# Optimization experiments

Hardware: AMD Instinct MI355X
Metric: run time of the kernel (lower is better)

## Reference

```python
import jax, jax.numpy as jnp
import numpy as np

B, N_BOX, N_THING, ROI = 2, 32, 4, 28
H, W = 768, 704
N_STUFF = 6
N_CLS = N_STUFF + N_THING  # 10
NEG = -100.0


def setup_inputs() -> dict:
    key = jax.random.key(0)
    k1, k2, k3, k4 = jax.random.split(key, 4)
    sem_logits = jax.random.normal(k1, (B, N_CLS, H, W), jnp.float32)
    roi_msk_logits = jax.random.normal(k2, (B, N_BOX, N_THING, ROI, ROI), jnp.float32)
    cls = jax.random.randint(k3, (B, N_BOX), 0, N_THING, jnp.int32)
    u = jax.random.uniform(k4, (B, N_BOX, 4), jnp.float32)
    y0 = u[..., 0] * (H - 80.0)
    x0 = u[..., 1] * (W - 80.0)
    y1 = jnp.minimum(y0 + 32.0 + u[..., 2] * (H / 3.0), H - 1.0)
    x1 = jnp.minimum(x0 + 32.0 + u[..., 3] * (W / 3.0), W - 1.0)
    bbx = jnp.stack([y0, x0, y1, x1], axis=-1)  # (y_min, x_min, y_max, x_max)
    img_size = jnp.array([H, W], jnp.int32)
    return {"sem_logits": sem_logits, "roi_msk_logits": roi_msk_logits,
            "bbx": bbx, "cls": cls, "img_size": img_size}


def _bilinear_paste(msk, bbx, img_size, Hs, Ws):
    # msk: [B,N,R,R]; per-box bilinear resize (align_corners=False) to (h,w) and paste
    # into a [B,N,Hs,Ws] canvas filled with -100, clipped to the image.
    R = msk.shape[-1]
    ref = jnp.floor(bbx).astype(jnp.int32)  # torch .long()/int() truncation (boxes >= 0)
    y0, x0, y1, x1 = ref[..., 0], ref[..., 1], ref[..., 2], ref[..., 3]
    h = jnp.maximum(y1 - y0 + 1, 1).astype(jnp.float32)
    w = jnp.maximum(x1 - x0 + 1, 1).astype(jnp.float32)
    yy = jnp.arange(Hs, dtype=jnp.float32)[None, None, :]          # [1,1,H]
    sy = jnp.clip((yy - y0[..., None] + 0.5) * (R / h)[..., None] - 0.5, 0.0, R - 1.0)
    ylo = jnp.floor(sy).astype(jnp.int32)
    yhi = jnp.minimum(ylo + 1, R - 1)
    wy = sy - ylo                                                   # [B,N,H]
    xx = jnp.arange(Ws, dtype=jnp.float32)[None, None, :]
    sx = jnp.clip((xx - x0[..., None] + 0.5) * (R / w)[..., None] - 0.5, 0.0, R - 1.0)
    xlo = jnp.floor(sx).astype(jnp.int32)
    xhi = jnp.minimum(xlo + 1, R - 1)
    wx = sx - xlo                                                   # [B,N,W]
    rows = (jnp.take_along_axis(msk, ylo[..., None], axis=2) * (1.0 - wy[..., None])
            + jnp.take_along_axis(msk, yhi[..., None], axis=2) * wy[..., None])  # [B,N,H,R]
    up = (jnp.take_along_axis(rows, xlo[:, :, None, :], axis=3) * (1.0 - wx[:, :, None, :])
          + jnp.take_along_axis(rows, xhi[:, :, None, :], axis=3) * wx[:, :, None, :])  # [B,N,H,W]
    yi = jnp.arange(Hs, dtype=jnp.int32)[None, None, :]
    xi = jnp.arange(Ws, dtype=jnp.int32)[None, None, :]
    in_y = (yi >= jnp.maximum(y0, 0)[..., None]) & (yi < jnp.minimum(y1 + 1, img_size[0])[..., None])
    in_x = (xi >= jnp.maximum(x0, 0)[..., None]) & (xi < jnp.minimum(x1 + 1, img_size[1])[..., None])
    inside = in_y[..., :, None] & in_x[..., None, :]
    return jnp.where(inside, up, NEG)


def _fused_logits(sem_logits, roi_msk_logits, bbx, cls, img_size):
    Bs, _, Hs, Ws = sem_logits.shape
    Nb = cls.shape[1]
    # gather per-box mask logits for its predicted thing class: [B,N,R,R]
    msk = roi_msk_logits[jnp.arange(Bs)[:, None], jnp.arange(Nb)[None, :], cls]
    po_mask = _bilinear_paste(msk, bbx, img_size, Hs, Ws)          # [B,N,H,W]
    # semantic-logit crops per box (po_sem_stride = 1)
    iy0 = jnp.floor(bbx[..., 0]).astype(jnp.int32)
    ix0 = jnp.floor(bbx[..., 1]).astype(jnp.int32)
    iy1 = (jnp.round(bbx[..., 2]) + 1.0).astype(jnp.int32)
    ix1 = (jnp.round(bbx[..., 3]) + 1.0).astype(jnp.int32)
    yi = jnp.arange(Hs, dtype=jnp.int32)[None, None, :]
    xi = jnp.arange(Ws, dtype=jnp.int32)[None, None, :]
    in2 = (((yi >= iy0[..., None]) & (yi < iy1[..., None]))[..., :, None]
           & ((xi >= ix0[..., None]) & (xi < ix1[..., None]))[..., None, :])
    sem_sel = sem_logits[:, N_STUFF:][jnp.arange(Bs)[:, None], cls]  # [B,N,H,W]
    po_inst = jnp.where(in2, sem_sel, NEG)
    combined = (jax.nn.sigmoid(po_inst) + jax.nn.sigmoid(po_mask)) * (po_inst + po_mask)
    return jnp.concatenate([sem_logits[:, :N_STUFF], combined], axis=1)  # [B,6+N,H,W]


def _label_single(pp, sp, cl):
    # pp: panoptic argmax [H,W]; sp: semantic argmax [H,W]; cl: [N] thing classes
    Nb = cl.shape[0]
    is_inst = pp >= N_STUFF
    nmap = jnp.clip(pp - N_STUFF, 0, Nb - 1)
    # joint histogram counts[n, c] = #pixels with po_pred == 6+n and sem_pred == c
    key = jnp.where(is_inst, (pp - N_STUFF) * N_CLS + sp, Nb * N_CLS)
    counts = jnp.zeros(Nb * N_CLS + 1, jnp.int32).at[key.ravel()].add(1)[:Nb * N_CLS].reshape(Nb, N_CLS)
    present = counts.sum(1) > 0
    idx = jnp.cumsum(present.astype(jnp.int32)) - 1  # enumeration order of torch.unique ids
    maj = jnp.argmax(counts, axis=1).astype(jnp.int32)  # ties -> smallest class (matches unique+argmax)
    frac = counts.max(1).astype(jnp.float32) / jnp.maximum(counts.sum(1), 1).astype(jnp.float32)
    thing = cl.astype(jnp.int32) + N_STUFF
    match = maj == thing
    to_stuff = (~match) & (frac >= 0.5) & (maj < N_STUFF)
    sem_val = jnp.where(to_stuff, maj, thing)
    inst_val = jnp.where(to_stuff, -1, idx)
    po_sem = jnp.where(is_inst, sem_val[nmap], pp)
    po_inst = jnp.where(is_inst, inst_val[nmap], -1)
    # po_min_stuff_area = 0 (default) -> stuff-area filter is a no-op
    sh = jnp.zeros(N_STUFF + 1, jnp.int32).at[jnp.where(po_sem < N_STUFF, po_sem, N_STUFF).ravel()].add(1)[:N_STUFF]
    s_present = sh > 0
    s_rank = jnp.cumsum(s_present.astype(jnp.int32)) - 1
    n_stuff = s_present.astype(jnp.int32).sum()
    ih = jnp.zeros(Nb + 1, jnp.int32).at[jnp.where(po_inst >= 0, po_inst, Nb).ravel()].add(1)[:Nb]
    i_present = ih > 0
    i_rank = jnp.cumsum(i_present.astype(jnp.int32)) - 1
    seam = jnp.where((po_inst < 0) & (po_sem < N_STUFF),
                     1 + s_rank[jnp.clip(po_sem, 0, N_STUFF - 1)], 0)
    seam = jnp.where(po_inst >= 0, 1 + n_stuff + i_rank[jnp.clip(po_inst, 0, Nb - 1)], seam)
    L = 1 + N_STUFF + Nb  # fixed-size padded po_cls (torch version is variable-length)
    cls_out = jnp.full(L, 255, jnp.int32)
    cls_out = cls_out.at[jnp.where(s_present, 1 + s_rank, L)].set(
        jnp.arange(N_STUFF, dtype=jnp.int32), mode='drop')
    inst_sem = jnp.full(Nb, 255, jnp.int32).at[
        jnp.where(present & (~to_stuff), idx, Nb)].set(sem_val.astype(jnp.int32), mode='drop')
    cls_out = cls_out.at[jnp.where(i_present, 1 + n_stuff + i_rank, L)].set(inst_sem, mode='drop')
    return seam.astype(jnp.int32), cls_out, jnp.zeros(L, jnp.int32)


def reference(sem_logits, roi_msk_logits, bbx, cls, img_size):
    logits = _fused_logits(sem_logits, roi_msk_logits, bbx, cls, img_size)
    po_pred = jnp.argmax(logits, axis=1)        # softmax is monotone -> argmax of logits
    sem_pred = jnp.argmax(sem_logits, axis=1)
    seam, po_cls, po_iscrowd = jax.vmap(_label_single)(po_pred, sem_pred, cls)
    Bs, Hs, Ws = seam.shape
    return seam.reshape(Bs * Hs, Ws), po_cls.reshape(-1), po_iscrowd.reshape(-1)
```

## Files before the change

kernel.cpp:

```cpp
#include <hip/hip_runtime.h>
#include <math.h>

#define NSTUFF 6
#define NCLS   10
#define NBOX   32
#define NTHING 4
#define RR     28
#define HH     768
#define WW     704
#define NPIX   (HH * WW)
#define BB     2
#define LL     (1 + NSTUFF + NBOX)
#define NEGV   (-100.0f)

#define TW 64
#define TH 16
#define TILES_X (WW / TW)
#define TILES_Y (HH / TH)
#define NTILES  (TILES_X * TILES_Y)
#define NHIST   (NBOX * NCLS + NSTUFF)
#define NTHR    1024

__device__ __forceinline__ float sigmoidf_(float x) {
    return 1.0f / (1.0f + expf(-x));
}

__global__ __launch_bounds__(NTHR, 4) void k_fuse(
    const float* __restrict__ sem,
    const float* __restrict__ roi,
    const float* __restrict__ bbx,
    const int*   __restrict__ cls,
    unsigned char* __restrict__ pred8,
    int*         __restrict__ counts,
    int*         __restrict__ stuffh)
{
    const int b = blockIdx.y;
    __shared__ int   sh_y0[NBOX], sh_x0[NBOX], sh_yme[NBOX], sh_xme[NBOX];
    __shared__ int   sh_yie[NBOX], sh_xie[NBOX], sh_moff[NBOX], sh_cls[NBOX];
    __shared__ float sh_y0f[NBOX], sh_x0f[NBOX], sh_sy[NBOX], sh_sx[NBOX];
    __shared__ int   sh_list[NBOX];
    __shared__ int   sh_nbox;
    __shared__ int   sh_cnt[NHIST];

    const int t = threadIdx.x;
    const int tile = blockIdx.x;
    const int tx0 = (tile % TILES_X) * TW;
    const int ty0 = (tile / TILES_X) * TH;

    const int x = tx0 + (t & 63);
    const int y = ty0 + (t >> 6);
    const int p = y * WW + x;

    const float* semb = sem + (size_t)b * NCLS * NPIX;
    float s[NCLS];
    #pragma unroll
    for (int c = 0; c < NCLS; ++c)
        s[c] = semb[(size_t)c * NPIX + p];

    for (int i = t; i < NHIST; i += NTHR) sh_cnt[i] = 0;

    if (t < 64) {
        bool flag = false;
        if (t < NBOX) {
            const float* bbp = bbx + ((size_t)b * NBOX + t) * 4;
            float y0f = bbp[0], x0f = bbp[1], y1f = bbp[2], x1f = bbp[3];
            int y0 = (int)floorf(y0f), x0 = (int)floorf(x0f);
            int y1 = (int)floorf(y1f), x1 = (int)floorf(x1f);
            int yme = min(y1 + 1, HH), xme = min(x1 + 1, WW);
            int yie = (int)rintf(y1f) + 1, xie = (int)rintf(x1f) + 1;
            sh_y0[t] = y0;  sh_x0[t] = x0;
            sh_yme[t] = yme; sh_xme[t] = xme;
            sh_yie[t] = yie; sh_xie[t] = xie;
            sh_y0f[t] = (float)y0; sh_x0f[t] = (float)x0;
            float hh = (float)max(y1 - y0 + 1, 1);
            float ww = (float)max(x1 - x0 + 1, 1);
            sh_sy[t] = 28.0f / hh;  sh_sx[t] = 28.0f / ww;
            int c = cls[b * NBOX + t];
            sh_cls[t] = c;
            sh_moff[t] = (((b * NBOX + t) * NTHING) + c) * (RR * RR);
            int uy = max(yme, yie), ux = max(xme, xie);
            flag = (y0 < ty0 + TH) && (uy > ty0) && (x0 < tx0 + TW) && (ux > tx0);
        }
        unsigned long long m = __ballot(flag);
        if (flag) {
            int pos = __popcll(m & (((unsigned long long)1 << t) - 1ull));
            sh_list[pos] = t;
        }
        if (t == 0) sh_nbox = __popcll(m);
    }
    __syncthreads();

    const int nb = sh_nbox;
    const float yf = (float)y, xf = (float)x;

    int   a_n = 0, a_c = 0;     bool a_inm = false, a_ini = false;
    float a_wy = 0.f, a_wx = 0.f, a_m00 = 0.f, a_m01 = 0.f, a_m10 = 0.f, a_m11 = 0.f;
    int   b_n = 0, b_c = 0;     bool b_inm = false, b_ini = false;
    float b_wy = 0.f, b_wx = 0.f, b_m00 = 0.f, b_m01 = 0.f, b_m10 = 0.f, b_m11 = 0.f;

#define STAGE_A(P, jj)                                                         \
    {                                                                          \
        const int n_ = sh_list[jj];                                            \
        P##_n = n_;                                                            \
        P##_c = sh_cls[n_];                                                    \
        P##_inm = (y >= max(sh_y0[n_], 0)) & (y < sh_yme[n_]) &                \
                  (x >= max(sh_x0[n_], 0)) & (x < sh_xme[n_]);                 \
        P##_ini = (y >= sh_y0[n_]) & (y < sh_yie[n_]) &                        \
                  (x >= sh_x0[n_]) & (x < sh_xie[n_]);                         \
        float sy_ = __fsub_rn(__fmul_rn(__fadd_rn(__fsub_rn(yf, sh_y0f[n_]), 0.5f), sh_sy[n_]), 0.5f); \
        sy_ = fminf(fmaxf(sy_, 0.0f), 27.0f);                                  \
        int ylo_ = (int)sy_;                                                   \
        int yhi_ = min(ylo_ + 1, RR - 1);                                      \
        P##_wy = __fsub_rn(sy_, (float)ylo_);                                  \
        float sx_ = __fsub_rn(__fmul_rn(__fadd_rn(__fsub_rn(xf, sh_x0f[n_]), 0.5f), sh_sx[n_]), 0.5f); \
        sx_ = fminf(fmaxf(sx_, 0.0f), 27.0f);                                  \
        int xlo_ = (int)sx_;                                                   \
        int xhi_ = min(xlo_ + 1, RR - 1);                                      \
        P##_wx = __fsub_rn(sx_, (float)xlo_);                                  \
        const float* m_ = roi + sh_moff[n_];                                   \
        P##_m00 = m_[ylo_ * RR + xlo_]; P##_m01 = m_[ylo_ * RR + xhi_];        \
        P##_m10 = m_[yhi_ * RR + xlo_]; P##_m11 = m_[yhi_ * RR + xhi_];        \
    }

#define STAGE_B(P)                                                             \
    {                                                                          \
        const int n_ = P##_n;                                                  \
        if (n_ > prev + 1 && bv < 0.0f) { bv = -0.0f; bi = NSTUFF + prev + 1; }\
        float v_;                                                              \
        if (P##_inm | P##_ini) {                                               \
            float pm_ = NEGV;                                                  \
            if (P##_inm) {                                                     \
                float omy_ = __fsub_rn(1.0f, P##_wy), omx_ = __fsub_rn(1.0f, P##_wx); \
                float rl_ = __fadd_rn(__fmul_rn(P##_m00, omy_), __fmul_rn(P##_m10, P##_wy)); \
                float rh_ = __fadd_rn(__fmul_rn(P##_m01, omy_), __fmul_rn(P##_m11, P##_wy)); \
                pm_ = __fadd_rn(__fmul_rn(rl_, omx_), __fmul_rn(rh_, P##_wx)); \
            }                                                                  \
            float pi_ = NEGV;                                                  \
            if (P##_ini) {                                                     \
                int c_ = P##_c;                                                \
                pi_ = (c_ == 0) ? s[6] : (c_ == 1) ? s[7] : (c_ == 2) ? s[8] : s[9]; \
            }                                                                  \
            v_ = __fmul_rn(__fadd_rn(sigmoidf_(pi_), sigmoidf_(pm_)), __fadd_rn(pi_, pm_)); \
        } else {                                                               \
            v_ = -0.0f;                                                        \
        }                                                                      \
        if (v_ > bv) { bv = v_; bi = NSTUFF + n_; }                            \
        prev = n_;                                                             \
    }

    if (nb > 0) STAGE_A(a, 0);

    float sb = s[0]; int sp = 0;
    #pragma unroll
    for (int c = 1; c < NCLS; ++c) if (s[c] > sb) { sb = s[c]; sp = c; }

    float bv = s[0]; int bi = 0;
    #pragma unroll
    for (int c = 1; c < NSTUFF; ++c) if (s[c] > bv) { bv = s[c]; bi = c; }

    int prev = -1;
    for (int jb = 0; jb < nb; ++jb) {
        if (jb + 1 < nb) STAGE_A(b, jb + 1);
        STAGE_B(a);
        a_n = b_n; a_c = b_c; a_inm = b_inm; a_ini = b_ini;
        a_wy = b_wy; a_wx = b_wx;
        a_m00 = b_m00; a_m01 = b_m01; a_m10 = b_m10; a_m11 = b_m11;
    }
    if (prev < NBOX - 1 && bv < 0.0f) { bi = NSTUFF + prev + 1; }

#undef STAGE_A
#undef STAGE_B

    pred8[(size_t)b * NPIX + p] = (unsigned char)bi;

    const int lane = t & 63;
    #pragma unroll
    for (int sc = 0; sc < NSTUFF; ++sc) {
        int c = __popcll(__ballot(bi == sc));
        if (lane == 0 && c) atomicAdd(&sh_cnt[NBOX * NCLS + sc], c);
    }
    if (bi >= NSTUFF) atomicAdd(&sh_cnt[(bi - NSTUFF) * NCLS + sp], 1);

    __syncthreads();
    for (int i = t; i < NHIST; i += NTHR) {
        int v = sh_cnt[i];
        if (v) {
            if (i < NBOX * NCLS) atomicAdd(&counts[b * NBOX * NCLS + i], v);
            else                 atomicAdd(&stuffh[b * NSTUFF + (i - NBOX * NCLS)], v);
        }
    }
}

__global__ __launch_bounds__(256) void k_relabel(
    const int*    __restrict__ counts,
    const int*    __restrict__ stuffh,
    const int*    __restrict__ cls,
    const uchar4* __restrict__ pred8,
    int*          __restrict__ out)
{
    const int b = blockIdx.y;
    const int t = threadIdx.x;
    __shared__ int slut[NSTUFF + NBOX];
    __shared__ int l_sh[NSTUFF];
    __shared__ int l_ih[NBOX];
    __shared__ int l_isem[NBOX];
    __shared__ int l_co[LL];

    const size_t q = (size_t)b * (NPIX / 4) + (size_t)blockIdx.x * 256 + t;
    const uchar4 v = pred8[q];

    int  ssum = 0, mj = 0, semv = 0, idx = -1;
    bool pres = false, ts = false;

    if (t < 64) {
        if (t < NSTUFF) l_sh[t] = stuffh[b * NSTUFF + t];
        if (t < NBOX)  { l_ih[t] = 0; l_isem[t] = 255; }
        if (t < LL)      l_co[t] = 255;

        if (t < NBOX) {
            const int* C = counts + ((size_t)b * NBOX + t) * NCLS;
            int c[NCLS];
            #pragma unroll
            for (int i = 0; i < NCLS; ++i) c[i] = C[i];
            int m = c[0]; mj = 0; ssum = c[0];
            #pragma unroll
            for (int i = 1; i < NCLS; ++i) {
                ssum += c[i];
                if (c[i] > m) { m = c[i]; mj = i; }
            }
            pres = ssum > 0;
            int thing = cls[b * NBOX + t] + NSTUFF;
            ts = pres && (mj != thing) && (2 * m >= ssum) && (mj < NSTUFF);
            semv = ts ? mj : thing;
        }
        unsigned long long pm = __ballot(pres);
        idx = __popcll(pm & (((unsigned long long)2 << t) - 1ull)) - 1;

        if (t < NBOX && pres &&  ts) atomicAdd(&l_sh[mj], ssum);
        if (t < NBOX && pres && !ts) { atomicAdd(&l_ih[idx], ssum); l_isem[idx] = semv; }
    }
    __syncthreads();

    if (t < 64) {
        bool spres = (t < NSTUFF) && (l_sh[t] > 0);
        unsigned long long sm = __ballot(spres);
        const int nst = __popcll(sm);
        bool ipres = (t < NBOX) && (l_ih[t] > 0);
        unsigned long long im = __ballot(ipres);

        auto srank = [&](int c) { return __popcll(sm & (((unsigned long long)2 << c) - 1ull)) - 1; };
        auto irank = [&](int j) { return __popcll(im & (((unsigned long long)2 << j) - 1ull)) - 1; };

        if (t < NSTUFF) slut[t] = 1 + srank(t);
        if (t < NBOX) {
            int q2 = idx < 0 ? 0 : idx;
            slut[NSTUFF + t] = ts ? (1 + srank(mj)) : (1 + nst + irank(q2));
        }
        if (spres) l_co[1 + srank(t)] = t;
        if (ipres) l_co[1 + nst + irank(t)] = l_isem[t];
    }
    __syncthreads();

    int4 o;
    o.x = slut[v.x];
    o.y = slut[v.y];
    o.z = slut[v.z];
    o.w = slut[v.w];
    ((int4*)out)[q] = o;

    if (blockIdx.x == 0 && t < LL) {
        int* ocls = out + (size_t)BB * NPIX + b * LL;
        int* ocrd = out + (size_t)BB * NPIX + BB * LL + b * LL;
        ocls[t] = l_co[t];
        ocrd[t] = 0;
    }
}

extern "C" void kernel_launch(void* const* d_in, const int* in_sizes, int n_in,
                              void* d_out, int out_size, void* d_ws, size_t ws_size,
                              hipStream_t stream) {
    (void)in_sizes; (void)n_in; (void)out_size; (void)ws_size;
    const float* sem = (const float*)d_in[0];
    const float* roi = (const float*)d_in[1];
    const float* bbx = (const float*)d_in[2];
    const int*   cls = (const int*)d_in[3];
    int* out = (int*)d_out;

    int* counts = (int*)d_ws;
    int* stuffh = counts + BB * NBOX * NCLS;
    unsigned char* pred8 = (unsigned char*)(stuffh + BB * NSTUFF);

    hipMemsetAsync(d_ws, 0, (BB * NBOX * NCLS + BB * NSTUFF) * sizeof(int), stream);

    dim3 g1(NTILES, BB);
    k_fuse<<<g1, NTHR, 0, stream>>>(sem, roi, bbx, cls, pred8, counts, stuffh);
    dim3 g2(NPIX / 1024, BB);
    k_relabel<<<g2, 256, 0, stream>>>(counts, stuffh, cls, (const uchar4*)pred8, out);
}
```

Baseline: 103.2 us.

## Replace global histogram atomics with per-tile partials and last-block LUT build

Each fuse block writes its local histogram to a per-tile partials buffer instead of doing global atomics. A ticket counter stored in the output's iscrowd region identifies the last block per batch, which reduces the partials and computes the relabel LUT and class list once. The memset and the redundant per-block LUT computation in the relabel kernel are removed, so relabel only loads a precomputed LUT. The ticket counter relies on the output region starting at zero or at a multiple of NTILES and later being overwritten with zeros, which is fragile, and the last block's serial reduction over 528 tiles adds tail latency.

```diff
diff --git a/kernel.cpp b/kernel.cpp
--- a/kernel.cpp
+++ b/kernel.cpp
@@ -19,6 +19,7 @@
 #define TILES_Y (HH / TH)
 #define NTILES  (TILES_X * TILES_Y)
 #define NHIST   (NBOX * NCLS + NSTUFF)
+#define NHP     328
 #define NTHR    1024
 
 __device__ __forceinline__ float sigmoidf_(float x) {
@@ -31,8 +32,9 @@
     const float* __restrict__ bbx,
     const int*   __restrict__ cls,
     unsigned char* __restrict__ pred8,
-    int*         __restrict__ counts,
-    int*         __restrict__ stuffh)
+    int*         __restrict__ partials,
+    int*         __restrict__ lutws,
+    int*         __restrict__ out)
 {
     const int b = blockIdx.y;
     __shared__ int   sh_y0[NBOX], sh_x0[NBOX], sh_yme[NBOX], sh_xme[NBOX];
@@ -41,6 +43,9 @@
     __shared__ int   sh_list[NBOX];
     __shared__ int   sh_nbox;
     __shared__ int   sh_cnt[NHIST];
+    __shared__ int   sh_old;
+    __shared__ int   w_sh[NSTUFF], w_ih[NBOX], w_isem[NBOX], w_co[LL];
+    __shared__ int   w_slut[NSTUFF + NBOX];
 
     const int t = threadIdx.x;
     const int tile = blockIdx.x;
@@ -182,83 +187,93 @@
     if (bi >= NSTUFF) atomicAdd(&sh_cnt[(bi - NSTUFF) * NCLS + sp], 1);
 
     __syncthreads();
-    for (int i = t; i < NHIST; i += NTHR) {
-        int v = sh_cnt[i];
-        if (v) {
-            if (i < NBOX * NCLS) atomicAdd(&counts[b * NBOX * NCLS + i], v);
-            else                 atomicAdd(&stuffh[b * NSTUFF + (i - NBOX * NCLS)], v);
-        }
+
+    int* myp = partials + ((size_t)b * NTILES + tile) * NHP;
+    for (int i = t; i < NHIST; i += NTHR) myp[i] = sh_cnt[i];
+    __threadfence();
+    __syncthreads();
+    if (t == 0)
+        sh_old = atomicAdd(out + (size_t)BB * NPIX + BB * LL + b * LL, 1);
+    __syncthreads();
+
+    if (((unsigned)(sh_old + 1)) % NTILES == 0) {
+        __threadfence();
+        if (t < NHIST) {
+            int a = 0;
+            const int* pb = partials + (size_t)b * NTILES * NHP + t;
+            #pragma unroll 4
+            for (int j = 0; j < NTILES; ++j) a += pb[(size_t)j * NHP];
+            sh_cnt[t] = a;
+        }
+        __syncthreads();
+
+        int  ssum = 0, mj = 0, semv = 0, idx = -1;
+        bool pres = false, ts = false;
+        if (t < 64) {
+            if (t < NSTUFF) w_sh[t] = sh_cnt[NBOX * NCLS + t];
+            if (t < NBOX)  { w_ih[t] = 0; w_isem[t] = 255; }
+            if (t < LL)      w_co[t] = 255;
+
+            if (t < NBOX) {
+                int m = sh_cnt[t * NCLS]; mj = 0; ssum = m;
+                #pragma unroll
+                for (int i = 1; i < NCLS; ++i) {
+                    int ci = sh_cnt[t * NCLS + i];
+                    ssum += ci;
+                    if (ci > m) { m = ci; mj = i; }
+                }
+                pres = ssum > 0;
+                int thing = cls[b * NBOX + t] + NSTUFF;
+                ts = pres && (mj != thing) && (2 * m >= ssum) && (mj < NSTUFF);
+                semv = ts ? mj : thing;
+            }
+            unsigned long long pm = __ballot(pres);
+            idx = __popcll(pm & (((unsigned long long)2 << t) - 1ull)) - 1;
+
+            if (t < NBOX && pres &&  ts) atomicAdd(&w_sh[mj], ssum);
+            if (t < NBOX && pres && !ts) { atomicAdd(&w_ih[idx], ssum); w_isem[idx] = semv; }
+        }
+        __syncthreads();
+        if (t < 64) {
+            bool spres = (t < NSTUFF) && (w_sh[t] > 0);
+            unsigned long long sm = __ballot(spres);
+            const int nst = __popcll(sm);
+            bool ipres = (t < NBOX) && (w_ih[t] > 0);
+            unsigned long long im = __ballot(ipres);
+
+            auto srank = [&](int c) { return __popcll(sm & (((unsigned long long)2 << c) - 1ull)) - 1; };
+            auto irank = [&](int j) { return __popcll(im & (((unsigned long long)2 << j) - 1ull)) - 1; };
+
+            if (t < NSTUFF) w_slut[t] = 1 + srank(t);
+            if (t < NBOX) {
+                int q2 = idx < 0 ? 0 : idx;
+                w_slut[NSTUFF + t] = ts ? (1 + srank(mj)) : (1 + nst + irank(q2));
+            }
+            if (spres) w_co[1 + srank(t)] = t;
+            if (ipres) w_co[1 + nst + irank(t)] = w_isem[t];
+        }
+        __syncthreads();
+        int* lutb = lutws + b * 128;
+        if (t < NSTUFF + NBOX) lutb[t] = w_slut[t];
+        if (t < LL) lutb[64 + t] = w_co[t];
     }
 }
 
 __global__ __launch_bounds__(256) void k_relabel(
-    const int*    __restrict__ counts,
-    const int*    __restrict__ stuffh,
-    const int*    __restrict__ cls,
+    const int*    __restrict__ lutws,
     const uchar4* __restrict__ pred8,
     int*          __restrict__ out)
 {
     const int b = blockIdx.y;
     const int t = threadIdx.x;
     __shared__ int slut[NSTUFF + NBOX];
-    __shared__ int l_sh[NSTUFF];
-    __shared__ int l_ih[NBOX];
-    __shared__ int l_isem[NBOX];
     __shared__ int l_co[LL];
 
     const size_t q = (size_t)b * (NPIX / 4) + (size_t)blockIdx.x * 256 + t;
     const uchar4 v = pred8[q];
 
-    int  ssum = 0, mj = 0, semv = 0, idx = -1;
-    bool pres = false, ts = false;
-
-    if (t < 64) {
-        if (t < NSTUFF) l_sh[t] = stuffh[b * NSTUFF + t];
-        if (t < NBOX)  { l_ih[t] = 0; l_isem[t] = 255; }
-        if (t < LL)      l_co[t] = 255;
-
-        if (t < NBOX) {
-            const int* C = counts + ((size_t)b * NBOX + t) * NCLS;
-            int c[NCLS];
-            #pragma unroll
-            for (int i = 0; i < NCLS; ++i) c[i] = C[i];
-            int m = c[0]; mj = 0; ssum = c[0];
-            #pragma unroll
-            for (int i = 1; i < NCLS; ++i) {
-                ssum += c[i];
-                if (c[i] > m) { m = c[i]; mj = i; }
-            }
-            pres = ssum > 0;
-            int thing = cls[b * NBOX + t] + NSTUFF;
-            ts = pres && (mj != thing) && (2 * m >= ssum) && (mj < NSTUFF);
-            semv = ts ? mj : thing;
-        }
-        unsigned long long pm = __ballot(pres);
-        idx = __popcll(pm & (((unsigned long long)2 << t) - 1ull)) - 1;
-
-        if (t < NBOX && pres &&  ts) atomicAdd(&l_sh[mj], ssum);
-        if (t < NBOX && pres && !ts) { atomicAdd(&l_ih[idx], ssum); l_isem[idx] = semv; }
-    }
-    __syncthreads();
-
-    if (t < 64) {
-        bool spres = (t < NSTUFF) && (l_sh[t] > 0);
-        unsigned long long sm = __ballot(spres);
-        const int nst = __popcll(sm);
-        bool ipres = (t < NBOX) && (l_ih[t] > 0);
-        unsigned long long im = __ballot(ipres);
-
-        auto srank = [&](int c) { return __popcll(sm & (((unsigned long long)2 << c) - 1ull)) - 1; };
-        auto irank = [&](int j) { return __popcll(im & (((unsigned long long)2 << j) - 1ull)) - 1; };
-
-        if (t < NSTUFF) slut[t] = 1 + srank(t);
-        if (t < NBOX) {
-            int q2 = idx < 0 ? 0 : idx;
-            slut[NSTUFF + t] = ts ? (1 + srank(mj)) : (1 + nst + irank(q2));
-        }
-        if (spres) l_co[1 + srank(t)] = t;
-        if (ipres) l_co[1 + nst + irank(t)] = l_isem[t];
-    }
+    if (t < NSTUFF + NBOX) slut[t] = lutws[b * 128 + t];
+    if (t < LL)            l_co[t] = lutws[b * 128 + 64 + t];
     __syncthreads();
 
     int4 o;
@@ -286,14 +301,12 @@
     const int*   cls = (const int*)d_in[3];
     int* out = (int*)d_out;
 
-    int* counts = (int*)d_ws;
-    int* stuffh = counts + BB * NBOX * NCLS;
-    unsigned char* pred8 = (unsigned char*)(stuffh + BB * NSTUFF);
-
-    hipMemsetAsync(d_ws, 0, (BB * NBOX * NCLS + BB * NSTUFF) * sizeof(int), stream);
+    int* partials = (int*)d_ws;
+    int* lutws = partials + (size_t)BB * NTILES * NHP;
+    unsigned char* pred8 = (unsigned char*)(lutws + BB * 128);
 
     dim3 g1(NTILES, BB);
-    k_fuse<<<g1, NTHR, 0, stream>>>(sem, roi, bbx, cls, pred8, counts, stuffh);
+    k_fuse<<<g1, NTHR, 0, stream>>>(sem, roi, bbx, cls, pred8, partials, lutws, out);
     dim3 g2(NPIX / 1024, BB);
-    k_relabel<<<g2, 256, 0, stream>>>(counts, stuffh, cls, (const uchar4*)pred8, out);
+    k_relabel<<<g2, 256, 0, stream>>>(lutws, (const uchar4*)pred8, out);
 }
```

Result: slower. 393.1 us (+280.8%).
